# Performance work log

Measured on AMD Instinct MI355X. Metric: run time of the kernel, lower is better.

The kernel has to match this reference:

```python
import jax, jax.numpy as jnp
import numpy as np

B, N, CIN = 8, 4096, 64
S, K, C = 1024, 32, 128      # npoint, k, out_channels
J, DEPTH, H = 5, 2, 4
BETA, EPS = 0.05, 1e-5


def _fps(xyz, npoint):
    # farthest point sampling, deterministic start at index 0
    Bb, Nn = xyz.shape[0], xyz.shape[1]
    bidx = jnp.arange(Bb)

    def step(carry, _):
        dist, far = carry
        cen = xyz[bidx, far][:, None, :]              # [B,1,3]
        d = jnp.sum((xyz - cen) ** 2, -1)             # [B,N]
        dist = jnp.minimum(dist, d)
        nxt = jnp.argmax(dist, axis=1).astype(jnp.int32)
        return (dist, nxt), far

    init = (jnp.full((Bb, Nn), 1e10, xyz.dtype), jnp.zeros((Bb,), jnp.int32))
    _, idxs = jax.lax.scan(step, init, None, length=npoint)
    return idxs.T                                      # [B,npoint]


def _ln(x, g, b):
    mu = jnp.mean(x, -1, keepdims=True)
    v = jnp.mean((x - mu) ** 2, -1, keepdims=True)
    return (x - mu) * jax.lax.rsqrt(v + EPS) * g + b


def _forward(xyz, points, w1, g1, b1, w2, g2, b2, w3, g3, b3,
             ws, wb, alpha, wqkv, wo, ln1g, ln1b, ln2g, ln2b):
    gather = jax.vmap(lambda a, i: a[i])
    fps_idx = _fps(xyz, S)
    new_xyz = gather(xyz, fps_idx)                     # [B,S,3]
    # kNN: squared distances from centroids to all points
    d2 = (jnp.sum(new_xyz ** 2, -1)[:, :, None] + jnp.sum(xyz ** 2, -1)[:, None, :]
          - 2.0 * jnp.einsum('bsd,bnd->bsn', new_xyz, xyz))   # [B,S,N]
    idx = jax.lax.top_k(-d2, K)[1]                     # [B,S,K]
    flat = idx.reshape(B, S * K)
    gxyz = gather(xyz, flat).reshape(B, S, K, 3)
    gnorm = gxyz - new_xyz[:, :, None, :]              # relative coords
    gpts = gather(points, flat).reshape(B, S, K, CIN)
    h = jnp.concatenate([gnorm, gpts], -1)             # [B,S,K,67]
    # pointwise shared MLP (1x1 conv + BN(batch stats) + ReLU)
    for w, g, b in ((w1, g1, b1), (w2, g2, b2), (w3, g3, b3)):
        h = jnp.einsum('bskc,oc->bsko', h, w)
        m = jnp.mean(h, (0, 1, 2))
        v = jnp.var(h, (0, 1, 2))
        h = jax.nn.relu((h - m) * jax.lax.rsqrt(v + EPS) * g + b)
    P = B * S
    pf = h.reshape(P, K, C)
    px = gnorm.reshape(P, K, 3)
    # per-patch graph: Gaussian affinity, sigma = mean pairwise distance
    dd = jnp.sum((px[:, :, None] - px[:, None, :]) ** 2, -1)   # [P,K,K]
    sigma = jnp.mean(jnp.sqrt(dd + 1e-12), (1, 2))[:, None, None]
    A = jnp.exp(-dd / (2.0 * sigma ** 2 + 1e-12))
    dinv = jax.lax.rsqrt(jnp.sum(A, -1) + 1e-12)
    I = jnp.eye(K, dtype=pf.dtype)
    L = I - dinv[:, :, None] * A * dinv[:, None, :]
    # heat-kernel wavelets psi_j = exp(-s_j L), 4th-order Taylor
    psis = []
    for j in range(J):
        M = (-BETA * (2.0 ** j)) * L
        T = I + M
        acc = M
        for m in range(2, 5):
            acc = jnp.einsum('pkl,plm->pkm', acc, M) / m
            T = T + acc
        psis.append(T)
    hcur = pf
    for d in range(DEPTH):
        mix = jnp.zeros_like(hcur)
        for j in range(J):
            mix = mix + alpha[d, j] * jnp.einsum('pkl,plc,cd->pkd', psis[j], hcur, ws[d, j])
        hcur = _ln(hcur + jax.nn.relu(mix + wb[d]), ln1g[d], ln1b[d])
        qkv = (hcur @ wqkv[d]).reshape(P, K, 3, H, C // H)
        q, k_, v = qkv[:, :, 0], qkv[:, :, 1], qkv[:, :, 2]      # [P,K,H,dh]
        att = jax.nn.softmax(jnp.einsum('pkhd,plhd->phkl', q, k_) / np.sqrt(C // H).astype(np.float32), axis=-1)
        o = jnp.einsum('phkl,plhd->pkhd', att, v).reshape(P, K, C) @ wo[d]
        hcur = _ln(hcur + o, ln2g[d], ln2b[d])
    out = jnp.max(hcur.reshape(B, S, K, C), axis=2)    # max-pool over k
    return new_xyz, out


def setup_inputs() -> dict:
    key = jax.random.key(0)
    ks = jax.random.split(key, 10)
    nrm = lambda k, shp, sc: jax.random.normal(k, shp, jnp.float32) * sc
    cin = CIN + 3
    return {
        'xyz': jax.random.normal(ks[0], (B, N, 3), jnp.float32),
        'points': jax.random.normal(ks[1], (B, N, CIN), jnp.float32),
        'w1': nrm(ks[2], (64, cin), cin ** -0.5),
        'g1': jnp.ones((64,)), 'b1': jnp.zeros((64,)),
        'w2': nrm(ks[3], (64, 64), 64 ** -0.5),
        'g2': jnp.ones((64,)), 'b2': jnp.zeros((64,)),
        'w3': nrm(ks[4], (C, 64), 64 ** -0.5),
        'g3': jnp.ones((C,)), 'b3': jnp.zeros((C,)),
        'ws': nrm(ks[5], (DEPTH, J, C, C), C ** -0.5),
        'wb': jnp.zeros((DEPTH, C)),
        'alpha': jnp.ones((DEPTH, J)) / J,
        'wqkv': nrm(ks[6], (DEPTH, C, 3 * C), C ** -0.5),
        'wo': nrm(ks[7], (DEPTH, C, C), C ** -0.5),
        'ln1g': jnp.ones((DEPTH, C)), 'ln1b': jnp.zeros((DEPTH, C)),
        'ln2g': jnp.ones((DEPTH, C)), 'ln2b': jnp.zeros((DEPTH, C)),
    }


def reference(xyz, points, w1, g1, b1, w2, g2, b2, w3, g3, b3,
              ws, wb, alpha, wqkv, wo, ln1g, ln1b, ln2g, ln2b):
    return _forward(xyz, points, w1, g1, b1, w2, g2, b2, w3, g3, b3,
                    ws, wb, alpha, wqkv, wo, ln1g, ln1b, ln2g, ln2b)
```

## Files before the change

### kernel.cpp

```cpp
#include <hip/hip_runtime.h>
#include <math.h>

#define NB 8
#define NP 4096
#define NCIN 64
#define NS 1024
#define NK 32
#define NC 128
#define NJ 5
#define NDEPTH 2
#define NH 4
#define NPTS (NB*NS)
#define NM (NPTS*NK)
#define EPSF 1e-5f

typedef float f32x4 __attribute__((ext_vector_type(4)));
typedef short bf16x8 __attribute__((ext_vector_type(8)));
typedef unsigned short ushort_t;
typedef unsigned long long u64;

#define MFMA(a,b,c) __builtin_amdgcn_mfma_f32_16x16x32_bf16(a,b,c,0,0,0)

__device__ __forceinline__ ushort_t f2b(float f) {
  unsigned int u = __float_as_uint(f);
  u = (u + 0x7fffu + ((u >> 16) & 1u)) >> 16;
  return (ushort_t)u;
}
__device__ __forceinline__ float b2f(ushort_t h) {
  unsigned int u = ((unsigned int)h) << 16;
  return __uint_as_float(u);
}

template<int CTRL>
__device__ __forceinline__ float dpp_f(float v) {
  return __int_as_float(__builtin_amdgcn_update_dpp(0, __float_as_int(v), CTRL, 0xf, 0xf, true));
}
__device__ __forceinline__ float dpp_sum16(float v) {
  v += dpp_f<0xB1>(v); v += dpp_f<0x4E>(v);
  v += dpp_f<0x141>(v); v += dpp_f<0x140>(v);
  return v;
}
__device__ __forceinline__ float dpp_max16(float v) {
  v = fmaxf(v, dpp_f<0xB1>(v)); v = fmaxf(v, dpp_f<0x4E>(v));
  v = fmaxf(v, dpp_f<0x141>(v)); v = fmaxf(v, dpp_f<0x140>(v));
  return v;
}

#define DPPMAX(CTRL) { \
  unsigned lo2 = (unsigned)__builtin_amdgcn_update_dpp(0, (int)(unsigned)best, CTRL, 0xf, 0xf, true); \
  unsigned hi2 = (unsigned)__builtin_amdgcn_update_dpp(0, (int)(unsigned)(best >> 32), CTRL, 0xf, 0xf, true); \
  u64 o = ((u64)hi2 << 32) | lo2; \
  if (o > best) best = o; }

__global__ __launch_bounds__(256) void k_fps(const float* __restrict__ xyz,
                                             float* __restrict__ newxyz) {
  const int b = blockIdx.x;
  const int t = threadIdx.x;
  const int lane = t & 63;
  const int w = t >> 6;
  __shared__ float Xl[NP*3];
  __shared__ float cenL[NS*3];
  __shared__ u64 slotP[2][4];
  __shared__ __align__(16) float slotC[2][4][4];
  const float* X = xyz + (size_t)b * NP * 3;
  for (int i = t; i < NP*3; i += 256) Xl[i] = X[i];
  __syncthreads();
  float px[16], py[16], pz[16], dist[16];
  unsigned inv[16];
#pragma unroll
  for (int i = 0; i < 16; ++i) {
    int n = t + 256*i;
    px[i] = Xl[3*n]; py[i] = Xl[3*n+1]; pz[i] = Xl[3*n+2];
    dist[i] = 1e10f;
    inv[i] = ~(unsigned)n;
  }
  float cx = Xl[0], cy = Xl[1], cz = Xl[2];
  for (int s = 0; s < NS; ++s) {
    if (t == 0) { cenL[3*s] = cx; cenL[3*s+1] = cy; cenL[3*s+2] = cz; }
    u64 pk[16];
#pragma unroll
    for (int i = 0; i < 16; ++i) {
      float dx = px[i]-cx, dy = py[i]-cy, dz = pz[i]-cz;
      float d = fmaf(dx,dx, fmaf(dy,dy, dz*dz));
      float nd = fminf(dist[i], d);
      dist[i] = nd;
      pk[i] = ((u64)__float_as_uint(nd) << 32) | inv[i];
    }
#pragma unroll
    for (int st = 1; st < 16; st <<= 1)
#pragma unroll
      for (int i = 0; i < 16; i += 2*st)
        pk[i] = pk[i+st] > pk[i] ? pk[i+st] : pk[i];
    u64 best = pk[0];
    DPPMAX(0x111)
    DPPMAX(0x112)
    DPPMAX(0x114)
    DPPMAX(0x118)
    DPPMAX(0x142)
    DPPMAX(0x143)
    if (lane == 63) {
      slotP[s&1][w] = best;
      int bi3 = 3 * (int)(~(unsigned)best);
      slotC[s&1][w][0] = Xl[bi3];
      slotC[s&1][w][1] = Xl[bi3+1];
      slotC[s&1][w][2] = Xl[bi3+2];
    }
    __syncthreads();
    const int par = s & 1;
    u64 s0 = slotP[par][0], s1 = slotP[par][1], s2 = slotP[par][2], s3 = slotP[par][3];
    f32x4 c0v = *(const f32x4*)&slotC[par][0][0];
    f32x4 c1v = *(const f32x4*)&slotC[par][1][0];
    f32x4 c2v = *(const f32x4*)&slotC[par][2][0];
    f32x4 c3v = *(const f32x4*)&slotC[par][3][0];
    u64 m = s0; f32x4 cw = c0v;
    if (s1 > m) { m = s1; cw = c1v; }
    if (s2 > m) { m = s2; cw = c2v; }
    if (s3 > m) { m = s3; cw = c3v; }
    cx = cw[0]; cy = cw[1]; cz = cw[2];
  }
  __syncthreads();
  float* o = newxyz + (size_t)b * NS * 3;
  for (int i = t; i < NS*3; i += 256) o[i] = cenL[i];
}

__global__ __launch_bounds__(64) void k_knn(const float* __restrict__ xyz,
                                            const float* __restrict__ newxyz,
                                            int* __restrict__ knn_idx,
                                            float* __restrict__ gnorm) {
  const int p = blockIdx.x;
  const int b = p >> 10;
  const int lane = threadIdx.x;
  const float* X = xyz + (size_t)b * NP * 3;
  __shared__ float d2[NP];
  float cx = newxyz[3*p], cy = newxyz[3*p+1], cz = newxyz[3*p+2];
  float sc = cx*cx + cy*cy + cz*cz;
#pragma unroll 4
  for (int i = 0; i < NP/64; ++i) {
    int n = lane + 64*i;
    float x = X[3*n], y = X[3*n+1], z = X[3*n+2];
    float sx = x*x + y*y + z*z;
    float dot = cx*x + cy*y + cz*z;
    d2[n] = sc + sx - 2.0f*dot;
  }
  for (int it = 0; it < NK; ++it) {
    float bv = 3.0e38f; int bi = 0x7fffffff;
#pragma unroll 8
    for (int i = 0; i < NP/64; ++i) {
      int n = lane + 64*i;
      float v = d2[n];
      if (v < bv) { bv = v; bi = n; }
    }
#pragma unroll
    for (int off = 32; off; off >>= 1) {
      float ov = __shfl_xor(bv, off);
      int   oi = __shfl_xor(bi, off);
      if (ov < bv || (ov == bv && oi < bi)) { bv = ov; bi = oi; }
    }
    if (lane == 0) {
      d2[bi] = 3.3e38f;
      knn_idx[p*NK + it] = bi;
      float* g = gnorm + ((size_t)p*NK + it)*3;
      g[0] = X[3*bi]   - cx;
      g[1] = X[3*bi+1] - cy;
      g[2] = X[3*bi+2] - cz;
    }
  }
}

__global__ __launch_bounds__(256) void k_layer1(const float* __restrict__ points,
                                                const int* __restrict__ knn_idx,
                                                const float* __restrict__ gnorm,
                                                const float* __restrict__ w1,
                                                float* __restrict__ y,
                                                float* __restrict__ stats) {
  const int r0 = blockIdx.x * 64;
  const int t = threadIdx.x;
  __shared__ float Xs[64][69];
  __shared__ float Ws[64][69];
  __shared__ int nid[64];
  __shared__ float ps[4][64], pss[4][64];
  if (t < 64) nid[t] = knn_idx[r0 + t];
  __syncthreads();
  for (int idx = t; idx < 64*67; idx += 256) {
    int r = idx / 67, c = idx % 67;
    int row = r0 + r;
    float v;
    if (c < 3) v = gnorm[(size_t)row*3 + c];
    else {
      int bb = row >> 15;
      int n = nid[r];
      v = points[((size_t)bb*NP + n)*NCIN + (c-3)];
    }
    Xs[r][c] = v;
  }
  for (int idx = t; idx < 64*67; idx += 256) {
    int o = idx / 67, c = idx % 67;
    Ws[o][c] = w1[idx];
  }
  __syncthreads();
  const int col = t & 63;
  const int rb  = t >> 6;
  float s1 = 0.f, s2 = 0.f;
  for (int i = 0; i < 16; ++i) {
    int r = rb + 4*i;
    float acc = 0.f;
#pragma unroll
    for (int c = 0; c < 67; ++c) acc += Xs[r][c] * Ws[col][c];
    y[(size_t)(r0 + r)*64 + col] = acc;
    s1 += acc; s2 += acc*acc;
  }
  ps[rb][col] = s1; pss[rb][col] = s2;
  __syncthreads();
  if (t < 64) {
    float a = ps[0][t]+ps[1][t]+ps[2][t]+ps[3][t];
    float q = pss[0][t]+pss[1][t]+pss[2][t]+pss[3][t];
    atomicAdd(&stats[t], a);
    atomicAdd(&stats[64 + t], q);
  }
}

template <int COUT>
__global__ __launch_bounds__(256) void k_layer(const float* __restrict__ xin,
                                               const float* __restrict__ aff,
                                               const float* __restrict__ w,
                                               float* __restrict__ y,
                                               float* __restrict__ stats) {
  const int r0 = blockIdx.x * 64;
  const int t = threadIdx.x;
  __shared__ float Xs[64][65];
  __shared__ float Ws[COUT][65];
  __shared__ float sa[64], sb[64];
  constexpr int NTR = 256 / COUT;
  __shared__ float ps[NTR][COUT], pss[NTR][COUT];
  if (t < 64) { sa[t] = aff[t]; sb[t] = aff[64 + t]; }
  __syncthreads();
  for (int idx = t; idx < 64*64; idx += 256) {
    int r = idx >> 6, c = idx & 63;
    float v = xin[(size_t)r0*64 + idx];
    Xs[r][c] = fmaxf(sa[c]*v + sb[c], 0.0f);
  }
  for (int idx = t; idx < COUT*64; idx += 256) {
    int o = idx >> 6, c = idx & 63;
    Ws[o][c] = w[idx];
  }
  __syncthreads();
  const int col = t & (COUT-1);
  const int rb  = t / COUT;
  float s1 = 0.f, s2 = 0.f;
  for (int i = 0; i < 64/NTR; ++i) {
    int r = rb + NTR*i;
    float acc = 0.f;
#pragma unroll
    for (int c = 0; c < 64; ++c) acc += Xs[r][c] * Ws[col][c];
    y[(size_t)(r0 + r)*COUT + col] = acc;
    s1 += acc; s2 += acc*acc;
  }
  ps[rb][col] = s1; pss[rb][col] = s2;
  __syncthreads();
  if (t < COUT) {
    float a = 0.f, q = 0.f;
    for (int n = 0; n < NTR; ++n) { a += ps[n][t]; q += pss[n][t]; }
    atomicAdd(&stats[t], a);
    atomicAdd(&stats[COUT + t], q);
  }
}

__global__ void k_finalize(const float* __restrict__ stats, const float* __restrict__ g,
                           const float* __restrict__ b, float* __restrict__ aff, int cout) {
  int t = threadIdx.x;
  if (t < cout) {
    const float inv = 1.0f / (float)NM;
    float m = stats[t] * inv;
    float var = stats[cout + t] * inv - m*m;
    float a = g[t] * rsqrtf(var + EPSF);
    aff[t] = a;
    aff[cout + t] = b[t] - m * a;
  }
}

__global__ __launch_bounds__(256) void k_pack(const float* __restrict__ ws,
                                              const float* __restrict__ wqkv,
                                              const float* __restrict__ wo,
                                              ushort_t* __restrict__ wpk) {
  int gid = blockIdx.x*256 + threadIdx.x;
  const float* src; int N_; int rem;
  if (gid < 163840)      { int mat = gid >> 14; rem = gid & 16383; src = ws  + (size_t)mat*16384; N_ = 128; }
  else if (gid < 262144) { int g2 = gid - 163840; int d = g2/49152; rem = g2 - d*49152; src = wqkv + (size_t)d*49152; N_ = 384; }
  else                   { int g3 = gid - 262144; int d = g3 >> 14; rem = g3 & 16383;  src = wo  + (size_t)d*16384; N_ = 128; }
  int NTN = N_ >> 4;
  int tile = rem >> 9, r = rem & 511;
  int tk = tile / NTN, tn = tile % NTN;
  int lane2 = r >> 3, jj = r & 7;
  int k = tk*32 + (lane2 >> 4)*8 + jj;
  int n = tn*16 + (lane2 & 15);
  wpk[gid] = f2b(src[(size_t)k*N_ + n]);
}

__global__ __launch_bounds__(256, 3) void k_group(
    const float* __restrict__ h3, const float* __restrict__ aff3,
    const float* __restrict__ gnorm,
    const ushort_t* __restrict__ wpk,
    const float* __restrict__ wb, const float* __restrict__ alpha,
    const float* __restrict__ ln1g, const float* __restrict__ ln1b,
    const float* __restrict__ ln2g, const float* __restrict__ ln2b,
    float* __restrict__ out) {
  const int p = blockIdx.x;
  const int t = threadIdx.x;
  const int lane = t & 63;
  const int w = t >> 6;
  const int lo16 = lane & 15;
  const int hi4 = lane >> 4;

  __shared__ __align__(16) ushort_t hbS[NK*NC];
  __shared__ __align__(16) ushort_t psisS[5*32*40];
  __shared__ __align__(16) unsigned char scratch[27648];

  float*    ddAF = (float*)scratch;
  float*    pxF  = (float*)(scratch + 4224);
  float*    dinvF= (float*)(scratch + 4608);
  float*    sigF = (float*)(scratch + 4736);
  ushort_t* LbS  = (ushort_t*)(scratch + 4768);
  ushort_t* PmS  = (ushort_t*)(scratch + 7328);
  ushort_t* qS   = (ushort_t*)scratch;
  ushort_t* kS2  = (ushort_t*)(scratch + 8704);
  ushort_t* vTS  = (ushort_t*)(scratch + 17408);
  float*    rowStat = (float*)(scratch + 20480);

  const int c0 = 32*w + lo16, c1 = c0 + 16;

  if (t < 96) pxF[t] = gnorm[(size_t)p*96 + t];
  const float* h3p = h3 + (size_t)p*4096;
#pragma unroll
  for (int i = 0; i < 16; ++i) {
    int idx = t + 256*i;
    int c = idx & 127, row = idx >> 7;
    float v = fmaxf(aff3[c]*h3p[idx] + aff3[128+c], 0.f);
    int ha = ((row << 8) + (c << 1)) ^ ((row & 7) << 4);
    hbS[ha >> 1] = f2b(v);
  }
  float hc[2][2][4];
  {
    float ga0 = aff3[c0], gb0 = aff3[128+c0];
    float ga1 = aff3[c1], gb1 = aff3[128+c1];
#pragma unroll
    for (int mi = 0; mi < 2; ++mi)
#pragma unroll
      for (int r = 0; r < 4; ++r) {
        int row = mi*16 + hi4*4 + r;
        hc[mi][0][r] = fmaxf(ga0*h3p[row*NC + c0] + gb0, 0.f);
        hc[mi][1][r] = fmaxf(ga1*h3p[row*NC + c1] + gb1, 0.f);
      }
  }
  __syncthreads();
  for (int i = t; i < 1024; i += 256) {
    int k = i >> 5, l = i & 31;
    float dx = pxF[k*3]  -pxF[l*3];
    float dy = pxF[k*3+1]-pxF[l*3+1];
    float dz = pxF[k*3+2]-pxF[l*3+2];
    ddAF[k*33+l] = dx*dx + dy*dy + dz*dz;
  }
  __syncthreads();
  float part = 0.f;
  for (int i = t; i < 1024; i += 256) part += sqrtf(ddAF[(i>>5)*33 + (i&31)] + 1e-12f);
#pragma unroll
  for (int off = 32; off; off >>= 1) part += __shfl_xor(part, off);
  if (lane == 0) sigF[w] = part;
  __syncthreads();
  if (t == 0) {
    float sg = (sigF[0]+sigF[1]+sigF[2]+sigF[3]) * (1.0f/1024.0f);
    sigF[4] = 2.0f*sg*sg + 1e-12f;
  }
  __syncthreads();
  const float denom = sigF[4];
  for (int i = t; i < 1024; i += 256) {
    int k = i >> 5, l = i & 31;
    ddAF[k*33+l] = expf(-ddAF[k*33+l] / denom);
  }
  __syncthreads();
  if (t < 32) {
    float s = 0.f;
    for (int l = 0; l < 32; ++l) s += ddAF[t*33 + l];
    dinvF[t] = rsqrtf(s + 1e-12f);
  }
  __syncthreads();
  for (int i = t; i < 1024; i += 256) {
    int k = i >> 5, l = i & 31;
    float v = -(dinvF[k] * ddAF[k*33+l] * dinvF[l]);
    if (k == l) v += 1.0f;
    LbS[k*40+l] = f2b(v);
  }
  __syncthreads();
  {
    int mi2 = w >> 1, ni2 = w & 1;
    int arow = (mi2*16 + lo16)*80 + (hi4 << 4);
    int brow = (ni2*16 + lo16)*80 + (hi4 << 4);
    bf16x8 bfr = *(const bf16x8*)((const char*)LbS + brow);
#pragma unroll
    for (int m = 2; m <= 4; ++m) {
      const ushort_t* Asrc = (m == 2) ? LbS : (PmS + (m-3)*1280);
      bf16x8 afr = *(const bf16x8*)((const char*)Asrc + arow);
      f32x4 z = {0.f,0.f,0.f,0.f};
      f32x4 pv = MFMA(afr, bfr, z);
      int rb2 = mi2*16 + hi4*4;
      int cl = ni2*16 + lo16;
#pragma unroll
      for (int r = 0; r < 4; ++r) PmS[(m-2)*1280 + (rb2+r)*40 + cl] = f2b(pv[r]);
      __syncthreads();
    }
  }
  for (int i = t; i < 1024; i += 256) {
    int k = i >> 5, l = i & 31;
    float lb = b2f(LbS[k*40+l]);
    float p2 = b2f(PmS[k*40+l]);
    float p3 = b2f(PmS[1280 + k*40+l]);
    float p4 = b2f(PmS[2560 + k*40+l]);
    float diag = (k == l) ? 1.0f : 0.0f;
#pragma unroll
    for (int j = 0; j < NJ; ++j) {
      float sj = -0.05f * (float)(1 << j);
      float cc2 = 0.5f*sj*sj;
      float cc3 = cc2*sj*(1.0f/3.0f);
      float cc4 = cc3*sj*0.25f;
      psisS[j*1280 + k*40 + l] = f2b(diag + sj*lb + cc2*p2 + cc3*p3 + cc4*p4);
    }
  }

  for (int d = 0; d < NDEPTH; ++d) {
    f32x4 m00 = {0.f,0.f,0.f,0.f}, m01 = m00, m10 = m00, m11 = m00;
    for (int jp = 0; jp < 3; ++jp) {
      const int njp = (jp == 2) ? 1 : 2;
      __syncthreads();
      for (int jj = 0; jj < njp; ++jj) {
        int j = 2*jp + jj;
        ushort_t* HjS = (ushort_t*)scratch + jj*5120;
        const ushort_t* Wp = wpk + (size_t)(d*NJ + j)*16384;
        const float alj = alpha[d*NJ + j];
#pragma unroll
        for (int tni = 0; tni < 2; ++tni) {
          int tn = 2*w + tni;
          f32x4 acc0 = {0.f,0.f,0.f,0.f}, acc1 = acc0;
#pragma unroll
          for (int tk = 0; tk < 4; ++tk) {
            bf16x8 bfr = *(const bf16x8*)(Wp + ((tk*8 + tn) << 9) + (lane << 3));
            int row0 = lo16;
            int ba0 = ((row0 << 8) + (tk << 6) + (hi4 << 4)) ^ ((row0 & 7) << 4);
            bf16x8 a0 = *(const bf16x8*)((const char*)hbS + ba0);
            acc0 = MFMA(a0, bfr, acc0);
            int row1 = 16 + lo16;
            int ba1 = ((row1 << 8) + (tk << 6) + (hi4 << 4)) ^ ((row1 & 7) << 4);
            bf16x8 a1 = *(const bf16x8*)((const char*)hbS + ba1);
            acc1 = MFMA(a1, bfr, acc1);
          }
          int c = tn*16 + lo16;
          int rbase = hi4*4;
#pragma unroll
          for (int r = 0; r < 4; ++r) {
            HjS[c*40 + rbase + r]      = f2b(alj * acc0[r]);
            HjS[c*40 + 16 + rbase + r] = f2b(alj * acc1[r]);
          }
        }
      }
      __syncthreads();
      for (int jj = 0; jj < njp; ++jj) {
        int j = 2*jp + jj;
        const char* psj = (const char*)(psisS + j*1280);
        const char* HjB = (const char*)scratch + jj*10240;
        int koff = hi4 << 4;
        bf16x8 pa0 = *(const bf16x8*)(psj + lo16*80 + koff);
        bf16x8 pa1 = *(const bf16x8*)(psj + (16 + lo16)*80 + koff);
        bf16x8 hb0 = *(const bf16x8*)(HjB + c0*80 + koff);
        bf16x8 hb1 = *(const bf16x8*)(HjB + c1*80 + koff);
        m00 = MFMA(pa0, hb0, m00);
        m01 = MFMA(pa0, hb1, m01);
        m10 = MFMA(pa1, hb0, m10);
        m11 = MFMA(pa1, hb1, m11);
      }
    }
    float u[2][2][4];
    {
      float wb0 = wb[d*NC + c0], wb1 = wb[d*NC + c1];
#pragma unroll
      for (int r = 0; r < 4; ++r) {
        u[0][0][r] = hc[0][0][r] + fmaxf(m00[r] + wb0, 0.f);
        u[0][1][r] = hc[0][1][r] + fmaxf(m01[r] + wb1, 0.f);
        u[1][0][r] = hc[1][0][r] + fmaxf(m10[r] + wb0, 0.f);
        u[1][1][r] = hc[1][1][r] + fmaxf(m11[r] + wb1, 0.f);
      }
#pragma unroll
      for (int mi = 0; mi < 2; ++mi)
#pragma unroll
        for (int r = 0; r < 4; ++r) {
          float s = u[mi][0][r] + u[mi][1][r];
          float q = u[mi][0][r]*u[mi][0][r] + u[mi][1][r]*u[mi][1][r];
          s = dpp_sum16(s);
          q = dpp_sum16(q);
          if (lo16 == 0) {
            int row = mi*16 + hi4*4 + r;
            rowStat[row*8 + w*2]     = s;
            rowStat[row*8 + w*2 + 1] = q;
          }
        }
    }
    __syncthreads();
    {
      float g0 = ln1g[d*NC + c0], b0 = ln1b[d*NC + c0];
      float g1 = ln1g[d*NC + c1], b1 = ln1b[d*NC + c1];
#pragma unroll
      for (int mi = 0; mi < 2; ++mi)
#pragma unroll
        for (int r = 0; r < 4; ++r) {
          int row = mi*16 + hi4*4 + r;
          f32x4 a = *(const f32x4*)(rowStat + row*8);
          f32x4 bq = *(const f32x4*)(rowStat + row*8 + 4);
          float mu = (a[0]+a[2]+bq[0]+bq[2]) * (1.0f/128.0f);
          float ex2 = (a[1]+a[3]+bq[1]+bq[3]) * (1.0f/128.0f);
          float rs = rsqrtf(ex2 - mu*mu + EPSF);
          float h0 = (u[mi][0][r] - mu)*rs*g0 + b0;
          float h1 = (u[mi][1][r] - mu)*rs*g1 + b1;
          hc[mi][0][r] = h0; hc[mi][1][r] = h1;
          int ha0 = ((row << 8) + (c0 << 1)) ^ ((row & 7) << 4);
          int ha1 = ((row << 8) + (c1 << 1)) ^ ((row & 7) << 4);
          hbS[ha0 >> 1] = f2b(h0);
          hbS[ha1 >> 1] = f2b(h1);
        }
    }
    __syncthreads();
    const ushort_t* Wq = wpk + 163840 + (size_t)d*49152;
#pragma unroll
    for (int ti = 0; ti < 12; ++ti) {
      int tile = w + 4*ti;
      int mi = (tile >= 24) ? 1 : 0;
      int tn = tile - 24*mi;
      int comp = tn >> 3;
      int cb = (tn & 7) * 16;
      f32x4 acc = {0.f,0.f,0.f,0.f};
#pragma unroll
      for (int tk = 0; tk < 4; ++tk) {
        bf16x8 bfr = *(const bf16x8*)(Wq + ((tk*24 + tn) << 9) + (lane << 3));
        int row = mi*16 + lo16;
        int ba = ((row << 8) + (tk << 6) + (hi4 << 4)) ^ ((row & 7) << 4);
        bf16x8 a = *(const bf16x8*)((const char*)hbS + ba);
        acc = MFMA(a, bfr, acc);
      }
      int cl = cb + lo16;
      int rb2 = mi*16 + hi4*4;
      if (comp == 0) {
#pragma unroll
        for (int r = 0; r < 4; ++r) qS[(rb2+r)*136 + cl] = f2b(acc[r]);
      } else if (comp == 1) {
#pragma unroll
        for (int r = 0; r < 4; ++r) kS2[(rb2+r)*136 + cl] = f2b(acc[r]);
      } else {
#pragma unroll
        for (int r = 0; r < 4; ++r) vTS[cl*40 + rb2 + r] = f2b(acc[r]);
      }
    }
    __syncthreads();
    float scr[2][2][4];
#pragma unroll
    for (int ti = 0; ti < 2; ++ti) {
      int pi = w + 4*ti;
      int h = pi >> 1, mi = pi & 1;
      int koff = h*64 + (hi4 << 4);
      bf16x8 qa = *(const bf16x8*)((const char*)qS + (mi*16 + lo16)*272 + koff);
#pragma unroll
      for (int ni = 0; ni < 2; ++ni) {
        bf16x8 kb = *(const bf16x8*)((const char*)kS2 + (ni*16 + lo16)*272 + koff);
        f32x4 z = {0.f,0.f,0.f,0.f};
        f32x4 sv = MFMA(qa, kb, z);
#pragma unroll
        for (int r = 0; r < 4; ++r) scr[ti][ni][r] = sv[r] * 0.17677669529663687f;
      }
    }
    __syncthreads();
#pragma unroll
    for (int ti = 0; ti < 2; ++ti) {
      int pi = w + 4*ti;
      int h = pi >> 1, mi = pi & 1;
#pragma unroll
      for (int r = 0; r < 4; ++r) {
        float s0 = scr[ti][0][r], s1 = scr[ti][1][r];
        float mx = dpp_max16(fmaxf(s0, s1));
        float e0 = expf(s0 - mx), e1 = expf(s1 - mx);
        float sum = dpp_sum16(e0 + e1);
        float iv = 1.0f / sum;
        int row = mi*16 + hi4*4 + r;
        qS[row*136 + h*32 + lo16]      = f2b(e0*iv);
        qS[row*136 + h*32 + 16 + lo16] = f2b(e1*iv);
      }
    }
    __syncthreads();
#pragma unroll
    for (int ti = 0; ti < 4; ++ti) {
      int tile = w + 4*ti;
      int h = tile >> 2, mi = (tile >> 1) & 1, ni = tile & 1;
      bf16x8 aa = *(const bf16x8*)((const char*)qS + (mi*16 + lo16)*272 + h*64 + (hi4 << 4));
      bf16x8 vb = *(const bf16x8*)((const char*)vTS + (h*32 + ni*16 + lo16)*80 + (hi4 << 4));
      f32x4 z = {0.f,0.f,0.f,0.f};
      f32x4 ov = MFMA(aa, vb, z);
      int col = h*32 + ni*16 + lo16;
      int rb2 = mi*16 + hi4*4;
#pragma unroll
      for (int r = 0; r < 4; ++r) {
        int row = rb2 + r;
        int ha = ((row << 8) + (col << 1)) ^ ((row & 7) << 4);
        hbS[ha >> 1] = f2b(ov[r]);
      }
    }
    __syncthreads();
    const ushort_t* Wop = wpk + 262144 + (size_t)d*16384;
#pragma unroll
    for (int tni = 0; tni < 2; ++tni) {
      int tn = 2*w + tni;
      f32x4 acc0 = {0.f,0.f,0.f,0.f}, acc1 = acc0;
#pragma unroll
      for (int tk = 0; tk < 4; ++tk) {
        bf16x8 bfr = *(const bf16x8*)(Wop + ((tk*8 + tn) << 9) + (lane << 3));
        int row0 = lo16;
        int ba0 = ((row0 << 8) + (tk << 6) + (hi4 << 4)) ^ ((row0 & 7) << 4);
        bf16x8 a0 = *(const bf16x8*)((const char*)hbS + ba0);
        acc0 = MFMA(a0, bfr, acc0);
        int row1 = 16 + lo16;
        int ba1 = ((row1 << 8) + (tk << 6) + (hi4 << 4)) ^ ((row1 & 7) << 4);
        bf16x8 a1 = *(const bf16x8*)((const char*)hbS + ba1);
        acc1 = MFMA(a1, bfr, acc1);
      }
#pragma unroll
      for (int r = 0; r < 4; ++r) {
        u[0][tni][r] = hc[0][tni][r] + acc0[r];
        u[1][tni][r] = hc[1][tni][r] + acc1[r];
      }
    }
#pragma unroll
    for (int mi = 0; mi < 2; ++mi)
#pragma unroll
      for (int r = 0; r < 4; ++r) {
        float s = u[mi][0][r] + u[mi][1][r];
        float q = u[mi][0][r]*u[mi][0][r] + u[mi][1][r]*u[mi][1][r];
        s = dpp_sum16(s);
        q = dpp_sum16(q);
        if (lo16 == 0) {
          int row = mi*16 + hi4*4 + r;
          rowStat[row*8 + w*2]     = s;
          rowStat[row*8 + w*2 + 1] = q;
        }
      }
    __syncthreads();
    {
      float g0 = ln2g[d*NC + c0], b0 = ln2b[d*NC + c0];
      float g1 = ln2g[d*NC + c1], b1 = ln2b[d*NC + c1];
#pragma unroll
      for (int mi = 0; mi < 2; ++mi)
#pragma unroll
        for (int r = 0; r < 4; ++r) {
          int row = mi*16 + hi4*4 + r;
          f32x4 a = *(const f32x4*)(rowStat + row*8);
          f32x4 bq = *(const f32x4*)(rowStat + row*8 + 4);
          float mu = (a[0]+a[2]+bq[0]+bq[2]) * (1.0f/128.0f);
          float ex2 = (a[1]+a[3]+bq[1]+bq[3]) * (1.0f/128.0f);
          float rs = rsqrtf(ex2 - mu*mu + EPSF);
          float h0 = (u[mi][0][r] - mu)*rs*g0 + b0;
          float h1 = (u[mi][1][r] - mu)*rs*g1 + b1;
          hc[mi][0][r] = h0; hc[mi][1][r] = h1;
          int ha0 = ((row << 8) + (c0 << 1)) ^ ((row & 7) << 4);
          int ha1 = ((row << 8) + (c1 << 1)) ^ ((row & 7) << 4);
          hbS[ha0 >> 1] = f2b(h0);
          hbS[ha1 >> 1] = f2b(h1);
        }
    }
  }
  {
    float v0 = hc[0][0][0], v1 = hc[0][1][0];
#pragma unroll
    for (int r = 1; r < 4; ++r) { v0 = fmaxf(v0, hc[0][0][r]); v1 = fmaxf(v1, hc[0][1][r]); }
#pragma unroll
    for (int r = 0; r < 4; ++r) { v0 = fmaxf(v0, hc[1][0][r]); v1 = fmaxf(v1, hc[1][1][r]); }
    v0 = fmaxf(v0, __shfl_xor(v0, 16)); v0 = fmaxf(v0, __shfl_xor(v0, 32));
    v1 = fmaxf(v1, __shfl_xor(v1, 16)); v1 = fmaxf(v1, __shfl_xor(v1, 32));
    if (hi4 == 0) {
      out[(size_t)p*NC + c0] = v0;
      out[(size_t)p*NC + c1] = v1;
    }
  }
}

extern "C" void kernel_launch(void* const* d_in, const int* in_sizes, int n_in,
                              void* d_out, int out_size, void* d_ws, size_t ws_size,
                              hipStream_t stream) {
  const float* xyz    = (const float*)d_in[0];
  const float* points = (const float*)d_in[1];
  const float* w1     = (const float*)d_in[2];
  const float* g1     = (const float*)d_in[3];
  const float* b1     = (const float*)d_in[4];
  const float* w2     = (const float*)d_in[5];
  const float* g2     = (const float*)d_in[6];
  const float* b2     = (const float*)d_in[7];
  const float* w3     = (const float*)d_in[8];
  const float* g3     = (const float*)d_in[9];
  const float* b3     = (const float*)d_in[10];
  const float* wsW    = (const float*)d_in[11];
  const float* wb     = (const float*)d_in[12];
  const float* alpha  = (const float*)d_in[13];
  const float* wqkv   = (const float*)d_in[14];
  const float* wo     = (const float*)d_in[15];
  const float* ln1g   = (const float*)d_in[16];
  const float* ln1b   = (const float*)d_in[17];
  const float* ln2g   = (const float*)d_in[18];
  const float* ln2b   = (const float*)d_in[19];
  float* outp = (float*)d_out;

  float* wsf   = (float*)d_ws;
  float* gnorm = wsf;
  float* stats = wsf + 786432;
  float* aff   = wsf + 787200;
  int*   knn   = (int*)(wsf + 787968);
  ushort_t* wpk = (ushort_t*)(wsf + 787968);
  float* h2    = wsf + 1050112;
  float* hX    = wsf + 17827328;

  hipMemsetAsync(stats, 0, 768*sizeof(float), stream);
  k_fps<<<NB, 256, 0, stream>>>(xyz, outp);
  k_knn<<<NPTS, 64, 0, stream>>>(xyz, outp, knn, gnorm);
  k_layer1<<<NM/64, 256, 0, stream>>>(points, knn, gnorm, w1, hX, stats);
  k_pack<<<294912/256, 256, 0, stream>>>(wsW, wqkv, wo, wpk);
  k_finalize<<<1, 128, 0, stream>>>(stats, g1, b1, aff, 64);
  k_layer<64><<<NM/64, 256, 0, stream>>>(hX, aff, w2, h2, stats + 256);
  k_finalize<<<1, 128, 0, stream>>>(stats + 256, g2, b2, aff + 256, 64);
  k_layer<128><<<NM/64, 256, 0, stream>>>(h2, aff + 256, w3, hX, stats + 512);
  k_finalize<<<1, 128, 0, stream>>>(stats + 512, g3, b3, aff + 512, 128);
  k_group<<<NPTS, 256, 0, stream>>>(hX, aff + 512, gnorm, wpk, wb, alpha,
                                    ln1g, ln1b, ln2g, ln2b, outp + (size_t)NB*NS*3);
}
```

Baseline: 2.120 ms.

## Widen FPS kernel to 1024 threads and relax k_group occupancy bound

The farthest-point-sampling kernel now runs 1024 threads per batch with 4 points per thread instead of 256 threads with 16. This shortens each thread's serial distance-update and argmax work per iteration. In exchange, the cross-wave reduction now covers 16 slots, and the winning centroid coordinates are looked up from shared memory after the barrier rather than being staged by each wave. Separately, k_group's launch bounds change from 3 to 2 blocks per CU, giving it more registers per thread at the cost of occupancy.

Result: faster. 2.077 ms (-2.0%).

```diff
diff --git a/kernel.cpp b/kernel.cpp
--- a/kernel.cpp
+++ b/kernel.cpp
@@ -52,24 +52,23 @@
   u64 o = ((u64)hi2 << 32) | lo2; \
   if (o > best) best = o; }
 
-__global__ __launch_bounds__(256) void k_fps(const float* __restrict__ xyz,
-                                             float* __restrict__ newxyz) {
+__global__ __launch_bounds__(1024) void k_fps(const float* __restrict__ xyz,
+                                              float* __restrict__ newxyz) {
   const int b = blockIdx.x;
   const int t = threadIdx.x;
   const int lane = t & 63;
   const int w = t >> 6;
   __shared__ float Xl[NP*3];
   __shared__ float cenL[NS*3];
-  __shared__ u64 slotP[2][4];
-  __shared__ __align__(16) float slotC[2][4][4];
+  __shared__ u64 slotP[2][16];
   const float* X = xyz + (size_t)b * NP * 3;
-  for (int i = t; i < NP*3; i += 256) Xl[i] = X[i];
-  __syncthreads();
-  float px[16], py[16], pz[16], dist[16];
-  unsigned inv[16];
-#pragma unroll
-  for (int i = 0; i < 16; ++i) {
-    int n = t + 256*i;
+  for (int i = t; i < NP*3; i += 1024) Xl[i] = X[i];
+  __syncthreads();
+  float px[4], py[4], pz[4], dist[4];
+  unsigned inv[4];
+#pragma unroll
+  for (int i = 0; i < 4; ++i) {
+    int n = t + 1024*i;
     px[i] = Xl[3*n]; py[i] = Xl[3*n+1]; pz[i] = Xl[3*n+2];
     dist[i] = 1e10f;
     inv[i] = ~(unsigned)n;
@@ -77,50 +76,41 @@
   float cx = Xl[0], cy = Xl[1], cz = Xl[2];
   for (int s = 0; s < NS; ++s) {
     if (t == 0) { cenL[3*s] = cx; cenL[3*s+1] = cy; cenL[3*s+2] = cz; }
-    u64 pk[16];
-#pragma unroll
-    for (int i = 0; i < 16; ++i) {
+    u64 pk[4];
+#pragma unroll
+    for (int i = 0; i < 4; ++i) {
       float dx = px[i]-cx, dy = py[i]-cy, dz = pz[i]-cz;
       float d = fmaf(dx,dx, fmaf(dy,dy, dz*dz));
       float nd = fminf(dist[i], d);
       dist[i] = nd;
       pk[i] = ((u64)__float_as_uint(nd) << 32) | inv[i];
     }
-#pragma unroll
-    for (int st = 1; st < 16; st <<= 1)
-#pragma unroll
-      for (int i = 0; i < 16; i += 2*st)
-        pk[i] = pk[i+st] > pk[i] ? pk[i+st] : pk[i];
-    u64 best = pk[0];
+    pk[0] = pk[1] > pk[0] ? pk[1] : pk[0];
+    pk[2] = pk[3] > pk[2] ? pk[3] : pk[2];
+    u64 best = pk[2] > pk[0] ? pk[2] : pk[0];
     DPPMAX(0x111)
     DPPMAX(0x112)
     DPPMAX(0x114)
     DPPMAX(0x118)
     DPPMAX(0x142)
     DPPMAX(0x143)
-    if (lane == 63) {
-      slotP[s&1][w] = best;
-      int bi3 = 3 * (int)(~(unsigned)best);
-      slotC[s&1][w][0] = Xl[bi3];
-      slotC[s&1][w][1] = Xl[bi3+1];
-      slotC[s&1][w][2] = Xl[bi3+2];
-    }
+    if (lane == 63) slotP[s&1][w] = best;
     __syncthreads();
-    const int par = s & 1;
-    u64 s0 = slotP[par][0], s1 = slotP[par][1], s2 = slotP[par][2], s3 = slotP[par][3];
-    f32x4 c0v = *(const f32x4*)&slotC[par][0][0];
-    f32x4 c1v = *(const f32x4*)&slotC[par][1][0];
-    f32x4 c2v = *(const f32x4*)&slotC[par][2][0];
-    f32x4 c3v = *(const f32x4*)&slotC[par][3][0];
-    u64 m = s0; f32x4 cw = c0v;
-    if (s1 > m) { m = s1; cw = c1v; }
-    if (s2 > m) { m = s2; cw = c2v; }
-    if (s3 > m) { m = s3; cw = c3v; }
-    cx = cw[0]; cy = cw[1]; cz = cw[2];
+    const u64* sl = slotP[s&1];
+    u64 v[16];
+#pragma unroll
+    for (int i = 0; i < 16; ++i) v[i] = sl[i];
+#pragma unroll
+    for (int st = 1; st < 16; st <<= 1)
+#pragma unroll
+      for (int i = 0; i < 16; i += 2*st)
+        v[i] = v[i+st] > v[i] ? v[i+st] : v[i];
+    int far = (int)(~(unsigned)v[0]);
+    cx = Xl[3*far]; cy = Xl[3*far+1]; cz = Xl[3*far+2];
   }
   __syncthreads();
   float* o = newxyz + (size_t)b * NS * 3;
-  for (int i = t; i < NS*3; i += 256) o[i] = cenL[i];
+  for (int i = t; i < NS*3; i += 1024) o[i] = cenL[i];
 }
 
 __global__ __launch_bounds__(64) void k_knn(const float* __restrict__ xyz,
@@ -296,7 +286,7 @@
   wpk[gid] = f2b(src[(size_t)k*N_ + n]);
 }
 
-__global__ __launch_bounds__(256, 3) void k_group(
+__global__ __launch_bounds__(256, 2) void k_group(
     const float* __restrict__ h3, const float* __restrict__ aff3,
     const float* __restrict__ gnorm,
     const ushort_t* __restrict__ wpk,
@@ -719,7 +709,7 @@
   float* hX    = wsf + 17827328;
 
   hipMemsetAsync(stats, 0, 768*sizeof(float), stream);
-  k_fps<<<NB, 256, 0, stream>>>(xyz, outp);
+  k_fps<<<NB, 1024, 0, stream>>>(xyz, outp);
   k_knn<<<NPTS, 64, 0, stream>>>(xyz, outp, knn, gnorm);
   k_layer1<<<NM/64, 256, 0, stream>>>(points, knn, gnorm, w1, hX, stats);
   k_pack<<<294912/256, 256, 0, stream>>>(wsW, wqkv, wo, wpk);
```

## Use bf16 MFMA for pointwise MLP layers 2 and 3 with prepacked weights

Applied to the files above, without the earlier changes.

Replaces the scalar fp32 shared-memory matmul in MLP layers 2 and 3 with bf16 MFMA 16x16x32. Inputs are converted to bf16 in LDS, and the weights are pre-packed into the MFMA fragment layout by an extended pack kernel. The BN statistics are reduced with wave shuffles before the atomics. The k_group launch bound also drops from 3 to 2 waves per EU. The change cuts ALU and LDS cost for layers that together handle 262K rows, at the cost of bf16 rounding of the activations and weights.

Result: faster. 1.807 ms (-14.8%).

```diff
diff --git a/kernel.cpp b/kernel.cpp
--- a/kernel.cpp
+++ b/kernel.cpp
@@ -220,48 +220,65 @@
 }
 
 template <int COUT>
-__global__ __launch_bounds__(256) void k_layer(const float* __restrict__ xin,
-                                               const float* __restrict__ aff,
-                                               const float* __restrict__ w,
-                                               float* __restrict__ y,
-                                               float* __restrict__ stats) {
+__global__ __launch_bounds__(256) void k_layerM(const float* __restrict__ xin,
+                                                const float* __restrict__ aff,
+                                                const ushort_t* __restrict__ wp,
+                                                float* __restrict__ y,
+                                                float* __restrict__ stats) {
   const int r0 = blockIdx.x * 64;
   const int t = threadIdx.x;
-  __shared__ float Xs[64][65];
-  __shared__ float Ws[COUT][65];
+  const int lane = t & 63;
+  const int w = t >> 6;
+  const int lo16 = lane & 15;
+  const int hi4 = lane >> 4;
+  constexpr int NTN = COUT >> 4;
+  __shared__ __align__(16) ushort_t XbS[64*72];
   __shared__ float sa[64], sb[64];
-  constexpr int NTR = 256 / COUT;
-  __shared__ float ps[NTR][COUT], pss[NTR][COUT];
+  __shared__ float ps[4][COUT], pss[4][COUT];
   if (t < 64) { sa[t] = aff[t]; sb[t] = aff[64 + t]; }
   __syncthreads();
-  for (int idx = t; idx < 64*64; idx += 256) {
+#pragma unroll
+  for (int i = 0; i < 16; ++i) {
+    int idx = t + 256*i;
     int r = idx >> 6, c = idx & 63;
     float v = xin[(size_t)r0*64 + idx];
-    Xs[r][c] = fmaxf(sa[c]*v + sb[c], 0.0f);
-  }
-  for (int idx = t; idx < COUT*64; idx += 256) {
-    int o = idx >> 6, c = idx & 63;
-    Ws[o][c] = w[idx];
-  }
-  __syncthreads();
-  const int col = t & (COUT-1);
-  const int rb  = t / COUT;
-  float s1 = 0.f, s2 = 0.f;
-  for (int i = 0; i < 64/NTR; ++i) {
-    int r = rb + NTR*i;
-    float acc = 0.f;
-#pragma unroll
-    for (int c = 0; c < 64; ++c) acc += Xs[r][c] * Ws[col][c];
-    y[(size_t)(r0 + r)*COUT + col] = acc;
-    s1 += acc; s2 += acc*acc;
-  }
-  ps[rb][col] = s1; pss[rb][col] = s2;
+    XbS[r*72 + c] = f2b(fmaxf(sa[c]*v + sb[c], 0.0f));
+  }
+  __syncthreads();
+  const int arow = (w*16 + lo16)*72;
+  float s1[NTN], s2[NTN];
+#pragma unroll
+  for (int tn = 0; tn < NTN; ++tn) {
+    f32x4 acc = {0.f,0.f,0.f,0.f};
+#pragma unroll
+    for (int tk = 0; tk < 2; ++tk) {
+      bf16x8 a = *(const bf16x8*)(XbS + arow + tk*32 + hi4*8);
+      bf16x8 b = *(const bf16x8*)(wp + ((tk*NTN + tn) << 9) + (lane << 3));
+      acc = MFMA(a, b, acc);
+    }
+    int col = tn*16 + lo16;
+    int rbase = r0 + w*16 + hi4*4;
+    float a1 = 0.f, a2 = 0.f;
+#pragma unroll
+    for (int r = 0; r < 4; ++r) {
+      y[(size_t)(rbase + r)*COUT + col] = acc[r];
+      a1 += acc[r]; a2 += acc[r]*acc[r];
+    }
+    a1 += __shfl_xor(a1, 16); a1 += __shfl_xor(a1, 32);
+    a2 += __shfl_xor(a2, 16); a2 += __shfl_xor(a2, 32);
+    s1[tn] = a1; s2[tn] = a2;
+  }
+  if (hi4 == 0) {
+#pragma unroll
+    for (int tn = 0; tn < NTN; ++tn) {
+      ps[w][tn*16 + lo16]  = s1[tn];
+      pss[w][tn*16 + lo16] = s2[tn];
+    }
+  }
   __syncthreads();
   if (t < COUT) {
-    float a = 0.f, q = 0.f;
-    for (int n = 0; n < NTR; ++n) { a += ps[n][t]; q += pss[n][t]; }
-    atomicAdd(&stats[t], a);
-    atomicAdd(&stats[COUT + t], q);
+    atomicAdd(&stats[t],        ps[0][t]+ps[1][t]+ps[2][t]+ps[3][t]);
+    atomicAdd(&stats[COUT + t], pss[0][t]+pss[1][t]+pss[2][t]+pss[3][t]);
   }
 }
 
@@ -281,22 +298,42 @@
 __global__ __launch_bounds__(256) void k_pack(const float* __restrict__ ws,
                                               const float* __restrict__ wqkv,
                                               const float* __restrict__ wo,
+                                              const float* __restrict__ w2,
+                                              const float* __restrict__ w3,
                                               ushort_t* __restrict__ wpk) {
   int gid = blockIdx.x*256 + threadIdx.x;
-  const float* src; int N_; int rem;
-  if (gid < 163840)      { int mat = gid >> 14; rem = gid & 16383; src = ws  + (size_t)mat*16384; N_ = 128; }
-  else if (gid < 262144) { int g2 = gid - 163840; int d = g2/49152; rem = g2 - d*49152; src = wqkv + (size_t)d*49152; N_ = 384; }
-  else                   { int g3 = gid - 262144; int d = g3 >> 14; rem = g3 & 16383;  src = wo  + (size_t)d*16384; N_ = 128; }
-  int NTN = N_ >> 4;
-  int tile = rem >> 9, r = rem & 511;
-  int tk = tile / NTN, tn = tile % NTN;
-  int lane2 = r >> 3, jj = r & 7;
-  int k = tk*32 + (lane2 >> 4)*8 + jj;
-  int n = tn*16 + (lane2 & 15);
-  wpk[gid] = f2b(src[(size_t)k*N_ + n]);
-}
-
-__global__ __launch_bounds__(256, 3) void k_group(
+  if (gid < 294912) {
+    const float* src; int N_; int rem;
+    if (gid < 163840)      { int mat = gid >> 14; rem = gid & 16383; src = ws  + (size_t)mat*16384; N_ = 128; }
+    else if (gid < 262144) { int g2 = gid - 163840; int d = g2/49152; rem = g2 - d*49152; src = wqkv + (size_t)d*49152; N_ = 384; }
+    else                   { int g3 = gid - 262144; int d = g3 >> 14; rem = g3 & 16383;  src = wo  + (size_t)d*16384; N_ = 128; }
+    int NTN = N_ >> 4;
+    int tile = rem >> 9, r = rem & 511;
+    int tk = tile / NTN, tn = tile % NTN;
+    int lane2 = r >> 3, jj = r & 7;
+    int k = tk*32 + (lane2 >> 4)*8 + jj;
+    int n = tn*16 + (lane2 & 15);
+    wpk[gid] = f2b(src[(size_t)k*N_ + n]);
+  } else if (gid < 299008) {
+    int rem = gid - 294912;
+    int tile = rem >> 9, r = rem & 511;
+    int tk = tile >> 2, tn = tile & 3;
+    int lane2 = r >> 3, jj = r & 7;
+    int k = tk*32 + (lane2 >> 4)*8 + jj;
+    int n = tn*16 + (lane2 & 15);
+    wpk[gid] = f2b(w2[n*64 + k]);
+  } else if (gid < 307200) {
+    int rem = gid - 299008;
+    int tile = rem >> 9, r = rem & 511;
+    int tk = tile >> 3, tn = tile & 7;
+    int lane2 = r >> 3, jj = r & 7;
+    int k = tk*32 + (lane2 >> 4)*8 + jj;
+    int n = tn*16 + (lane2 & 15);
+    wpk[gid] = f2b(w3[n*64 + k]);
+  }
+}
+
+__global__ __launch_bounds__(256, 2) void k_group(
     const float* __restrict__ h3, const float* __restrict__ aff3,
     const float* __restrict__ gnorm,
     const ushort_t* __restrict__ wpk,
@@ -722,11 +759,11 @@
   k_fps<<<NB, 256, 0, stream>>>(xyz, outp);
   k_knn<<<NPTS, 64, 0, stream>>>(xyz, outp, knn, gnorm);
   k_layer1<<<NM/64, 256, 0, stream>>>(points, knn, gnorm, w1, hX, stats);
-  k_pack<<<294912/256, 256, 0, stream>>>(wsW, wqkv, wo, wpk);
+  k_pack<<<307200/256, 256, 0, stream>>>(wsW, wqkv, wo, w2, w3, wpk);
   k_finalize<<<1, 128, 0, stream>>>(stats, g1, b1, aff, 64);
-  k_layer<64><<<NM/64, 256, 0, stream>>>(hX, aff, w2, h2, stats + 256);
+  k_layerM<64><<<NM/64, 256, 0, stream>>>(hX, aff, wpk + 294912, h2, stats + 256);
   k_finalize<<<1, 128, 0, stream>>>(stats + 256, g2, b2, aff + 256, 64);
-  k_layer<128><<<NM/64, 256, 0, stream>>>(h2, aff + 256, w3, hX, stats + 512);
+  k_layerM<128><<<NM/64, 256, 0, stream>>>(h2, aff + 256, wpk + 299008, hX, stats + 512);
   k_finalize<<<1, 128, 0, stream>>>(stats + 512, g3, b3, aff + 512, 128);
   k_group<<<NPTS, 256, 0, stream>>>(hX, aff + 512, gnorm, wpk, wb, alpha,
                                     ln1g, ln1b, ln2g, ln2b, outp + (size_t)NB*NS*3);
```
